# Kernel tuning notes

Measured on AMD Instinct MI355X. Metric: run time of the kernel, lower is better.

## Reference

```python
import jax, jax.numpy as jnp
import numpy as np

BS, L, D = 32, 512, 512
N_CHARS = 32
DICT = 97

def setup_inputs() -> dict:
    key = jax.random.key(0)
    ks = jax.random.split(key, 10)
    s = 1.0 / np.sqrt(D)
    return {
        "inp": jax.random.normal(ks[0], (BS, L, D), jnp.float32),
        "emb": jax.random.normal(ks[1], (N_CHARS, D), jnp.float32) * 0.02,  # embedding table; char_orders == arange
        "Wo_w": jax.random.normal(ks[2], (D, D), jnp.float32) * s,
        "Wo_b": jnp.zeros((D,), jnp.float32),
        "Wv_w": jax.random.normal(ks[3], (D, D), jnp.float32) * s,
        "Wv_b": jnp.zeros((D,), jnp.float32),
        "We_w": jax.random.normal(ks[4], (D, 1), jnp.float32) * s,
        "We_b": jnp.zeros((1,), jnp.float32),
        "Wc_w": jax.random.normal(ks[5], (D, DICT), jnp.float32) * s,
        "Wc_b": jnp.zeros((DICT,), jnp.float32),
    }

def reference(inp, emb, Wo_w, Wo_b, Wv_w, Wv_b, We_w, We_b, Wc_w, Wc_b):
    # O = embedding(arange(max_n_chars)) is just the full embedding table: (n, d)
    w_o = emb @ Wo_w + Wo_b                      # (n, d)
    w_v = inp @ Wv_w + Wv_b                      # (b, L, d)
    # broadcast add -> tanh -> score projection: (b, n, L, d) -> (b, n, L)
    h = jnp.tanh(w_o[None, :, None, :] + w_v[:, None, :, :])
    e = jnp.einsum('bnld,d->bnl', h, We_w[:, 0]) + We_b[0]
    alpha = jax.nn.softmax(e, axis=2)            # softmax over L (axis=2)
    visual_features = jnp.einsum('bnl,bld->bnd', alpha, inp)  # (b, n, d)
    logits = visual_features @ Wc_w + Wc_b       # (b, n, dict)
    return (visual_features, logits)
```

## Files before the change

### kernel.cpp

```cpp
#include <hip/hip_runtime.h>
#include <hip/hip_bf16.h>

#define BS    32
#define LSEQ  512
#define DIM   512
#define NCH   32
#define NDICT 97
#define CHB   16

#define TANH_SCALE 2.8853900817779268f

typedef __attribute__((ext_vector_type(8))) short bf16x8;
typedef __attribute__((ext_vector_type(4))) float f32x4;

#define GLDS16(gsrc, ldst) \
  __builtin_amdgcn_global_load_lds((const __attribute__((address_space(1))) void*)(gsrc), \
                                   (__attribute__((address_space(3))) void*)(ldst), 16, 0, 0)

__device__ __forceinline__ float sig_from_scaled(float xs) {
    float e2 = __builtin_amdgcn_exp2f(xs);
    return __builtin_amdgcn_rcpf(1.0f + e2);
}

__device__ __forceinline__ void split2u(float x0, float x1, unsigned& hp, unsigned& lp) {
    unsigned r0 = __float_as_uint(x0) + 0x8000u;
    unsigned r1 = __float_as_uint(x1) + 0x8000u;
    float f0 = __uint_as_float(r0 & 0xFFFF0000u);
    float f1 = __uint_as_float(r1 & 0xFFFF0000u);
    hp = (r0 >> 16) | (r1 & 0xFFFF0000u);
    unsigned s0 = __float_as_uint(x0 - f0);
    unsigned s1 = __float_as_uint(x1 - f1);
    lp = (s0 >> 16) | (s1 & 0xFFFF0000u);
}

__global__ __launch_bounds__(256) void k_misc(
    const float* __restrict__ Wv, ushort* __restrict__ BhiT, ushort* __restrict__ BloT,
    const float* __restrict__ Wo, ushort* __restrict__ WohiT, ushort* __restrict__ WoloT,
    const float* __restrict__ emb, ushort* __restrict__ embH, ushort* __restrict__ embL)
{
    __shared__ float tile[64][65];
    const int bid = blockIdx.x;
    const int t = threadIdx.x;
    if (bid < 128) {
        const bool isWv = bid < 64;
        const float* src = isWv ? Wv : Wo;
        ushort* dH = isWv ? BhiT : WohiT;
        ushort* dL = isWv ? BloT : WoloT;
        const int bb = bid & 63;
        const int k0 = (bb >> 3) * 64, n0 = (bb & 7) * 64;
        const int tr = t >> 4, tc = (t & 15) * 4;
        #pragma unroll
        for (int rr = 0; rr < 64; rr += 16) {
            float4 v = *(const float4*)&src[(size_t)(k0 + rr + tr) * DIM + n0 + tc];
            tile[rr + tr][tc + 0] = v.x; tile[rr + tr][tc + 1] = v.y;
            tile[rr + tr][tc + 2] = v.z; tile[rr + tr][tc + 3] = v.w;
        }
        __syncthreads();
        #pragma unroll
        for (int rr = 0; rr < 64; rr += 16) {
            const int n = rr + tr;
            unsigned h01, l01, h23, l23;
            split2u(tile[tc + 0][n] * TANH_SCALE, tile[tc + 1][n] * TANH_SCALE, h01, l01);
            split2u(tile[tc + 2][n] * TANH_SCALE, tile[tc + 3][n] * TANH_SCALE, h23, l23);
            *(uint2*)&dH[(size_t)(n0 + n) * DIM + k0 + tc] = make_uint2(h01, h23);
            *(uint2*)&dL[(size_t)(n0 + n) * DIM + k0 + tc] = make_uint2(l01, l23);
        }
    } else {
        for (int i = t; i < 4096; i += 256) {
            float4 v = ((const float4*)emb)[i];
            unsigned h01, l01, h23, l23;
            split2u(v.x, v.y, h01, l01);
            split2u(v.z, v.w, h23, l23);
            ((uint2*)embH)[i] = make_uint2(h01, h23);
            ((uint2*)embL)[i] = make_uint2(l01, l23);
        }
    }
}

__global__ __launch_bounds__(256) void k_gemm(
    const float* __restrict__ A,
    const ushort* __restrict__ Bhi, const ushort* __restrict__ Blo,
    const float* __restrict__ bias, float* __restrict__ C,
    const ushort* __restrict__ WohiT, const ushort* __restrict__ WoloT,
    const ushort* __restrict__ embH, const ushort* __restrict__ embL,
    const float* __restrict__ Wo_b, float* __restrict__ w_o)
{
    __shared__ ushort Bh[128 * 64], Bl[128 * 64];

    const int bid = blockIdx.x;
    const int t = threadIdx.x;
    const int wave = t >> 6, lane = t & 63;
    const int rl = lane >> 3;
    const int gsw = (lane & 7) ^ rl;

    if (bid < 512) {
        const int mb = (bid & 7) * 16 + (bid >> 5);
        const int nb = (bid >> 3) & 3;
        const int bm = mb * 128, bn = nb * 128;
        const int wm = wave >> 1, wn = wave & 1;
        const int am = bm + wm * 64 + (lane & 15);
        const int ak = (lane >> 4) * 8;

        f32x4 acc[4][4] = {};

        for (int k0 = 0; k0 < DIM; k0 += 64) {
            bf16x8 ah[4][2], al[4][2];
            #pragma unroll
            for (int i = 0; i < 4; ++i)
                #pragma unroll
                for (int kh = 0; kh < 2; ++kh) {
                    const float* ap = A + (size_t)(am + i * 16) * DIM + k0 + kh * 32 + ak;
                    float4 v0 = *(const float4*)ap;
                    float4 v1 = *(const float4*)(ap + 4);
                    union { unsigned u[4]; bf16x8 v; } H, L;
                    split2u(v0.x, v0.y, H.u[0], L.u[0]);
                    split2u(v0.z, v0.w, H.u[1], L.u[1]);
                    split2u(v1.x, v1.y, H.u[2], L.u[2]);
                    split2u(v1.z, v1.w, H.u[3], L.u[3]);
                    ah[i][kh] = H.v; al[i][kh] = L.v;
                }
            #pragma unroll
            for (int c4 = 0; c4 < 4; ++c4) {
                const int c = wave * 4 + c4;
                const size_t rb = (size_t)(bn + c * 8 + rl) * DIM + k0 + gsw * 8;
                GLDS16(Bhi + rb, &Bh[c * 512]);
                GLDS16(Blo + rb, &Bl[c * 512]);
            }
            __syncthreads();

            #pragma unroll
            for (int kh = 0; kh < 2; ++kh) {
                const int p = ((kh * 4 + (lane >> 4)) ^ (lane & 7)) * 8;
                bf16x8 bh[4], bl[4];
                #pragma unroll
                for (int j = 0; j < 4; ++j) {
                    const int rbr = (wn * 64 + j * 16 + (lane & 15)) * 64 + p;
                    bh[j] = *(const bf16x8*)&Bh[rbr];
                    bl[j] = *(const bf16x8*)&Bl[rbr];
                }
                #pragma unroll
                for (int i = 0; i < 4; ++i)
                    #pragma unroll
                    for (int j = 0; j < 4; ++j) {
                        acc[i][j] = __builtin_amdgcn_mfma_f32_16x16x32_bf16(ah[i][kh], bh[j], acc[i][j], 0, 0, 0);
                        acc[i][j] = __builtin_amdgcn_mfma_f32_16x16x32_bf16(ah[i][kh], bl[j], acc[i][j], 0, 0, 0);
                        acc[i][j] = __builtin_amdgcn_mfma_f32_16x16x32_bf16(al[i][kh], bh[j], acc[i][j], 0, 0, 0);
                    }
            }
            __syncthreads();
        }

        #pragma unroll
        for (int i = 0; i < 4; ++i) {
            const int m = bm + wm * 64 + i * 16 + (lane >> 4) * 4;
            #pragma unroll
            for (int j = 0; j < 4; ++j) {
                const int n = bn + wn * 64 + j * 16 + (lane & 15);
                const float bb = TANH_SCALE * bias[n];
                #pragma unroll
                for (int r = 0; r < 4; ++r)
                    C[(size_t)(m + r) * DIM + n] = acc[i][j][r] + bb;
            }
        }
    } else {
        const int nb0 = (bid - 512) * 128;
        f32x4 acc[2][2] = {};

        for (int k0 = 0; k0 < DIM; k0 += 64) {
            bf16x8 eh[2][2], el[2][2];
            #pragma unroll
            for (int m = 0; m < 2; ++m)
                #pragma unroll
                for (int kh = 0; kh < 2; ++kh) {
                    const size_t ra = (size_t)(m * 16 + (lane & 15)) * DIM + k0 + kh * 32 + (lane >> 4) * 8;
                    eh[m][kh] = *(const bf16x8*)&embH[ra];
                    el[m][kh] = *(const bf16x8*)&embL[ra];
                }
            #pragma unroll
            for (int c4 = 0; c4 < 4; ++c4) {
                const int c = wave * 4 + c4;
                const size_t rb = (size_t)(nb0 + c * 8 + rl) * DIM + k0 + gsw * 8;
                GLDS16(WohiT + rb, &Bh[c * 512]);
                GLDS16(WoloT + rb, &Bl[c * 512]);
            }
            __syncthreads();

            #pragma unroll
            for (int kh = 0; kh < 2; ++kh) {
                const int p = ((kh * 4 + (lane >> 4)) ^ (lane & 7)) * 8;
                bf16x8 bh[2], bl[2];
                #pragma unroll
                for (int j = 0; j < 2; ++j) {
                    const int rbr = (wave * 32 + j * 16 + (lane & 15)) * 64 + p;
                    bh[j] = *(const bf16x8*)&Bh[rbr];
                    bl[j] = *(const bf16x8*)&Bl[rbr];
                }
                #pragma unroll
                for (int m = 0; m < 2; ++m)
                    #pragma unroll
                    for (int j = 0; j < 2; ++j) {
                        acc[m][j] = __builtin_amdgcn_mfma_f32_16x16x32_bf16(eh[m][kh], bh[j], acc[m][j], 0, 0, 0);
                        acc[m][j] = __builtin_amdgcn_mfma_f32_16x16x32_bf16(eh[m][kh], bl[j], acc[m][j], 0, 0, 0);
                        acc[m][j] = __builtin_amdgcn_mfma_f32_16x16x32_bf16(el[m][kh], bh[j], acc[m][j], 0, 0, 0);
                    }
            }
            __syncthreads();
        }

        #pragma unroll
        for (int m = 0; m < 2; ++m) {
            const int row = m * 16 + (lane >> 4) * 4;
            #pragma unroll
            for (int j = 0; j < 2; ++j) {
                const int col = nb0 + wave * 32 + j * 16 + (lane & 15);
                const float bb = TANH_SCALE * Wo_b[col];
                #pragma unroll
                for (int r = 0; r < 4; ++r)
                    w_o[(size_t)(row + r) * DIM + col] = acc[m][j][r] + bb;
            }
        }
    }
}

__global__ __launch_bounds__(256, 4) void k_e(
    const float* __restrict__ w_v, const float* __restrict__ w_o,
    const float* __restrict__ We_w, float* __restrict__ e)
{
    __shared__ float4 woS[CHB * 128];
    const int lblk = blockIdx.x;
    const int b    = blockIdx.y;
    const int ch0  = blockIdx.z * CHB;
    const int t    = threadIdx.x;

    const float4* wog = ((const float4*)w_o) + ch0 * (DIM / 4);
    #pragma unroll
    for (int i = 0; i < CHB * 128 / 256; ++i)
        woS[t + 256 * i] = wog[t + 256 * i];

    const int wave = t >> 6, lane = t & 63;
    const int g = lane >> 4, j = lane & 15;
    const int l = lblk * 16 + wave * 4 + g;

    const float4* wvp = (const float4*)(w_v + (size_t)(b * LSEQ + l) * DIM);
    const float4* wep = (const float4*)We_w;
    float4 wv[8], we[8];
    #pragma unroll
    for (int k = 0; k < 8; ++k) {
        wv[k] = wvp[16 * k + j];
        we[k] = wep[16 * k + j];
    }
    float wsum = 0.0f;
    #pragma unroll
    for (int k = 0; k < 8; ++k)
        wsum += (we[k].x + we[k].y) + (we[k].z + we[k].w);
    #pragma unroll
    for (int off = 1; off < 16; off <<= 1) wsum += __shfl_xor(wsum, off, 64);

    __syncthreads();

    float sv[CHB];
    #pragma unroll 4
    for (int i = 0; i < CHB; ++i) {
        const float4* wrow = &woS[i * 128];
        float s0 = 0.f, s1 = 0.f, s2 = 0.f, s3 = 0.f;
        #pragma unroll
        for (int k = 0; k < 8; ++k) {
            float4 wo4 = wrow[16 * k + j];
            s0 = fmaf(we[k].x, sig_from_scaled(wo4.x + wv[k].x), s0);
            s1 = fmaf(we[k].y, sig_from_scaled(wo4.y + wv[k].y), s1);
            s2 = fmaf(we[k].z, sig_from_scaled(wo4.z + wv[k].z), s2);
            s3 = fmaf(we[k].w, sig_from_scaled(wo4.w + wv[k].w), s3);
        }
        sv[i] = (s0 + s1) + (s2 + s3);
    }

    float t2[8];
    #pragma unroll
    for (int i = 0; i < 8; ++i) {
        float a = sv[2 * i]     + __shfl_xor(sv[2 * i],     1, 64);
        float c = sv[2 * i + 1] + __shfl_xor(sv[2 * i + 1], 1, 64);
        t2[i] = (j & 1) ? c : a;
    }
    float t4[4];
    #pragma unroll
    for (int i = 0; i < 4; ++i) {
        float a = t2[2 * i]     + __shfl_xor(t2[2 * i],     2, 64);
        float c = t2[2 * i + 1] + __shfl_xor(t2[2 * i + 1], 2, 64);
        t4[i] = (j & 2) ? c : a;
    }
    float t8[2];
    #pragma unroll
    for (int i = 0; i < 2; ++i) {
        float a = t4[2 * i]     + __shfl_xor(t4[2 * i],     4, 64);
        float c = t4[2 * i + 1] + __shfl_xor(t4[2 * i + 1], 4, 64);
        t8[i] = (j & 4) ? c : a;
    }
    float a = t8[0] + __shfl_xor(t8[0], 8, 64);
    float c = t8[1] + __shfl_xor(t8[1], 8, 64);
    float res = (j & 8) ? c : a;

    e[(size_t)(b * NCH + ch0 + j) * LSEQ + l] = fmaf(-2.0f, res, wsum);
}

__global__ __launch_bounds__(256) void k_soft(
    const float* __restrict__ e, ushort* __restrict__ aH, ushort* __restrict__ aL)
{
    const int row = blockIdx.x * 4 + (threadIdx.x >> 6);
    const int lane = threadIdx.x & 63;
    const float4* erow = (const float4*)(e + (size_t)row * LSEQ);
    float4 v0 = erow[2 * lane], v1 = erow[2 * lane + 1];
    float m = fmaxf(fmaxf(fmaxf(v0.x, v0.y), fmaxf(v0.z, v0.w)),
                    fmaxf(fmaxf(v1.x, v1.y), fmaxf(v1.z, v1.w)));
    #pragma unroll
    for (int off = 32; off > 0; off >>= 1) m = fmaxf(m, __shfl_xor(m, off, 64));
    float p[8];
    p[0] = __expf(v0.x - m); p[1] = __expf(v0.y - m);
    p[2] = __expf(v0.z - m); p[3] = __expf(v0.w - m);
    p[4] = __expf(v1.x - m); p[5] = __expf(v1.y - m);
    p[6] = __expf(v1.z - m); p[7] = __expf(v1.w - m);
    float s = ((p[0] + p[1]) + (p[2] + p[3])) + ((p[4] + p[5]) + (p[6] + p[7]));
    #pragma unroll
    for (int off = 32; off > 0; off >>= 1) s += __shfl_xor(s, off, 64);
    const float inv = 1.0f / s;
    unsigned h01, l01, h23, l23, h45, l45, h67, l67;
    split2u(p[0] * inv, p[1] * inv, h01, l01);
    split2u(p[2] * inv, p[3] * inv, h23, l23);
    split2u(p[4] * inv, p[5] * inv, h45, l45);
    split2u(p[6] * inv, p[7] * inv, h67, l67);
    uint2* oh = (uint2*)(aH + (size_t)row * LSEQ);
    uint2* ol = (uint2*)(aL + (size_t)row * LSEQ);
    oh[2 * lane]     = make_uint2(h01, h23);
    oh[2 * lane + 1] = make_uint2(h45, h67);
    ol[2 * lane]     = make_uint2(l01, l23);
    ol[2 * lane + 1] = make_uint2(l45, l67);
}

__global__ __launch_bounds__(256) void k_vf(
    const float* __restrict__ inp,
    const ushort* __restrict__ aH, const ushort* __restrict__ aL,
    float* __restrict__ part)
{
    __shared__ unsigned T[4][16 * 68];
    const int dgrp = blockIdx.x >> 1, ls = blockIdx.x & 1;
    const int b = blockIdx.y;
    const int t = threadIdx.x, wave = t >> 6, lane = t & 63;
    const int d0 = (dgrp * 4 + wave) * 16;
    const int lbase = ls * 256;
    const int c = lane & 15, g = lane >> 4;

    unsigned* Tw = T[wave];
    const ushort* aHb = aH + (size_t)b * NCH * LSEQ;
    const ushort* aLb = aL + (size_t)b * NCH * LSEQ;

    f32x4 acc0 = {}, acc1 = {};

    for (int l0 = 0; l0 < 256; l0 += 64) {
        const float4* src = (const float4*)(inp + ((size_t)(b * LSEQ) + lbase + l0 + lane) * DIM + d0);
        float4 v0 = src[0], v1 = src[1], v2 = src[2], v3 = src[3];
        unsigned ev[16];
        {
            unsigned hp, lp;
            split2u(v0.x, v0.y, hp, lp); ev[0] = (lp << 16) | (hp & 0xFFFFu); ev[1] = (lp & 0xFFFF0000u) | (hp >> 16);
            split2u(v0.z, v0.w, hp, lp); ev[2] = (lp << 16) | (hp & 0xFFFFu); ev[3] = (lp & 0xFFFF0000u) | (hp >> 16);
            split2u(v1.x, v1.y, hp, lp); ev[4] = (lp << 16) | (hp & 0xFFFFu); ev[5] = (lp & 0xFFFF0000u) | (hp >> 16);
            split2u(v1.z, v1.w, hp, lp); ev[6] = (lp << 16) | (hp & 0xFFFFu); ev[7] = (lp & 0xFFFF0000u) | (hp >> 16);
            split2u(v2.x, v2.y, hp, lp); ev[8] = (lp << 16) | (hp & 0xFFFFu); ev[9] = (lp & 0xFFFF0000u) | (hp >> 16);
            split2u(v2.z, v2.w, hp, lp); ev[10] = (lp << 16) | (hp & 0xFFFFu); ev[11] = (lp & 0xFFFF0000u) | (hp >> 16);
            split2u(v3.x, v3.y, hp, lp); ev[12] = (lp << 16) | (hp & 0xFFFFu); ev[13] = (lp & 0xFFFF0000u) | (hp >> 16);
            split2u(v3.z, v3.w, hp, lp); ev[14] = (lp << 16) | (hp & 0xFFFFu); ev[15] = (lp & 0xFFFF0000u) | (hp >> 16);
        }
        #pragma unroll
        for (int i = 0; i < 16; ++i)
            Tw[i * 68 + lane] = ev[i];
        #pragma unroll
        for (int ks = 0; ks < 2; ++ks) {
            const unsigned* bp = &Tw[c * 68 + ks * 32 + g * 8];
            uint4 w0 = *(const uint4*)bp;
            uint4 w1 = *(const uint4*)(bp + 4);
            union { unsigned u[4]; bf16x8 v; } H, L;
            H.u[0] = (w0.x & 0xFFFFu) | (w0.y << 16);
            H.u[1] = (w0.z & 0xFFFFu) | (w0.w << 16);
            H.u[2] = (w1.x & 0xFFFFu) | (w1.y << 16);
            H.u[3] = (w1.z & 0xFFFFu) | (w1.w << 16);
            L.u[0] = (w0.x >> 16) | (w0.y & 0xFFFF0000u);
            L.u[1] = (w0.z >> 16) | (w0.w & 0xFFFF0000u);
            L.u[2] = (w1.x >> 16) | (w1.y & 0xFFFF0000u);
            L.u[3] = (w1.z >> 16) | (w1.w & 0xFFFF0000u);

            const int lfrag = lbase + l0 + ks * 32 + g * 8;
            bf16x8 a0h = *(const bf16x8*)&aHb[(size_t)c * LSEQ + lfrag];
            bf16x8 a0l = *(const bf16x8*)&aLb[(size_t)c * LSEQ + lfrag];
            bf16x8 a1h = *(const bf16x8*)&aHb[(size_t)(16 + c) * LSEQ + lfrag];
            bf16x8 a1l = *(const bf16x8*)&aLb[(size_t)(16 + c) * LSEQ + lfrag];

            acc0 = __builtin_amdgcn_mfma_f32_16x16x32_bf16(a0h, H.v, acc0, 0, 0, 0);
            acc0 = __builtin_amdgcn_mfma_f32_16x16x32_bf16(a0h, L.v, acc0, 0, 0, 0);
            acc0 = __builtin_amdgcn_mfma_f32_16x16x32_bf16(a0l, H.v, acc0, 0, 0, 0);
            acc1 = __builtin_amdgcn_mfma_f32_16x16x32_bf16(a1h, H.v, acc1, 0, 0, 0);
            acc1 = __builtin_amdgcn_mfma_f32_16x16x32_bf16(a1h, L.v, acc1, 0, 0, 0);
            acc1 = __builtin_amdgcn_mfma_f32_16x16x32_bf16(a1l, H.v, acc1, 0, 0, 0);
        }
    }

    const size_t base = (size_t)(ls * BS * NCH + b * NCH) * DIM + d0 + c;
    #pragma unroll
    for (int r = 0; r < 4; ++r) {
        part[base + (size_t)(g * 4 + r) * DIM]        = acc0[r];
        part[base + (size_t)(16 + g * 4 + r) * DIM]   = acc1[r];
    }
}

__global__ __launch_bounds__(256) void k_lg(
    const float* __restrict__ part, const float* __restrict__ Wc_w,
    const float* __restrict__ Wc_b, float* __restrict__ out_vf,
    float* __restrict__ out_logits)
{
    __shared__ float vfS[4][DIM];
    __shared__ float lgS[2][4][NDICT];
    const int r0 = blockIdx.x * 4;
    const int t = threadIdx.x;
    const int wave = t >> 6, lane = t & 63;

    const float2* p0 = (const float2*)(part + (size_t)(r0 + wave) * DIM);
    const float2* p1 = (const float2*)(part + (size_t)(BS * NCH + r0 + wave) * DIM);
    float2* vout = (float2*)(out_vf + (size_t)(r0 + wave) * DIM);
    #pragma unroll
    for (int q = 0; q < 4; ++q) {
        float2 x = p0[lane + 64 * q], y = p1[lane + 64 * q];
        float2 z; z.x = x.x + y.x; z.y = x.y + y.y;
        ((float2*)&vfS[wave][0])[lane + 64 * q] = z;
        vout[lane + 64 * q] = z;
    }
    __syncthreads();

    const int j = t & 127, half = t >> 7;
    if (j < NDICT) {
        const float* wc = Wc_w + (size_t)half * 256 * NDICT + j;
        const float* v0 = &vfS[0][half * 256];
        const float* v1 = &vfS[1][half * 256];
        const float* v2 = &vfS[2][half * 256];
        const float* v3 = &vfS[3][half * 256];
        float a0 = 0.f, a1 = 0.f, a2 = 0.f, a3 = 0.f;
        #pragma unroll 4
        for (int d = 0; d < 256; ++d) {
            float w = wc[(size_t)d * NDICT];
            a0 = fmaf(v0[d], w, a0); a1 = fmaf(v1[d], w, a1);
            a2 = fmaf(v2[d], w, a2); a3 = fmaf(v3[d], w, a3);
        }
        lgS[half][0][j] = a0; lgS[half][1][j] = a1;
        lgS[half][2][j] = a2; lgS[half][3][j] = a3;
    }
    __syncthreads();
    for (int idx = t; idx < 4 * NDICT; idx += 256) {
        const int r = idx / NDICT, jj = idx - r * NDICT;
        out_logits[(size_t)(r0 + r) * NDICT + jj] = Wc_b[jj] + lgS[0][r][jj] + lgS[1][r][jj];
    }
}

extern "C" void kernel_launch(void* const* d_in, const int* in_sizes, int n_in,
                              void* d_out, int out_size, void* d_ws, size_t ws_size,
                              hipStream_t stream)
{
    const float* inp  = (const float*)d_in[0];
    const float* emb  = (const float*)d_in[1];
    const float* Wo_w = (const float*)d_in[2];
    const float* Wo_b = (const float*)d_in[3];
    const float* Wv_w = (const float*)d_in[4];
    const float* Wv_b = (const float*)d_in[5];
    const float* We_w = (const float*)d_in[6];
    const float* Wc_w = (const float*)d_in[8];
    const float* Wc_b = (const float*)d_in[9];

    char* p = (char*)d_ws;
    float*  w_o   = (float*)p;  p += (64 << 10);
    float*  ev    = (float*)p;  p += (size_t)BS * NCH * LSEQ * 4;
    ushort* BhiT  = (ushort*)p; p += (size_t)DIM * DIM * 2;
    ushort* BloT  = (ushort*)p; p += (size_t)DIM * DIM * 2;
    ushort* WohiT = (ushort*)p; p += (size_t)DIM * DIM * 2;
    ushort* WoloT = (ushort*)p; p += (size_t)DIM * DIM * 2;
    ushort* embH  = (ushort*)p; p += (size_t)NCH * DIM * 2;
    ushort* embL  = (ushort*)p; p += (size_t)NCH * DIM * 2;
    ushort* aH    = (ushort*)p; p += (size_t)BS * NCH * LSEQ * 2;
    ushort* aL    = (ushort*)p; p += (size_t)BS * NCH * LSEQ * 2;
    float*  partV = (float*)p;  p += (size_t)2 * BS * NCH * DIM * 4;
    float*  w_v   = (float*)p;

    float* out_vf = (float*)d_out;
    float* out_lg = out_vf + BS * NCH * DIM;

    k_misc<<<dim3(129), dim3(256), 0, stream>>>(Wv_w, BhiT, BloT, Wo_w, WohiT, WoloT, emb, embH, embL);
    k_gemm<<<dim3(516), dim3(256), 0, stream>>>(inp, BhiT, BloT, Wv_b, w_v,
                                                WohiT, WoloT, embH, embL, Wo_b, w_o);
    k_e<<<dim3(LSEQ / 16, BS, NCH / CHB), dim3(256), 0, stream>>>(w_v, w_o, We_w, ev);
    k_soft<<<dim3(256), dim3(256), 0, stream>>>(ev, aH, aL);
    k_vf<<<dim3(16, BS), dim3(256), 0, stream>>>(inp, aH, aL, partV);
    k_lg<<<dim3(256), dim3(256), 0, stream>>>(partV, Wc_w, Wc_b, out_vf, out_lg);
}
```

Before: 175.1 us.

## Pre-split input into bf16 hi/lo planes and stage A tiles via LDS

Adds a separate kernel that splits the fp32 input into bf16 hi/lo arrays once. The GEMM then loads both A and B tiles into LDS with direct global-to-LDS loads and a new XOR swizzle, using a 32-wide K step instead of 64. This removes per-block fp32 loading and splitting of A, which was repeated across the four N-blocks, and moves A staging onto the async LDS path. In exchange it adds an extra pass that writes and re-reads about 32 MB of hi/lo data, and it halves the work done per barrier.

```diff
diff --git a/kernel.cpp b/kernel.cpp
--- a/kernel.cpp
+++ b/kernel.cpp
@@ -31,6 +31,22 @@
     unsigned s0 = __float_as_uint(x0 - f0);
     unsigned s1 = __float_as_uint(x1 - f1);
     lp = (s0 >> 16) | (s1 & 0xFFFF0000u);
+}
+
+__global__ __launch_bounds__(256) void k_prep_a(
+    const float* __restrict__ in, ushort* __restrict__ hi, ushort* __restrict__ lo)
+{
+    const int i0 = blockIdx.x * 1024 + threadIdx.x;
+    #pragma unroll
+    for (int rep = 0; rep < 4; ++rep) {
+        const int i = i0 + rep * 256;
+        float4 v = ((const float4*)in)[i];
+        unsigned h01, l01, h23, l23;
+        split2u(v.x, v.y, h01, l01);
+        split2u(v.z, v.w, h23, l23);
+        ((uint2*)hi)[i] = make_uint2(h01, h23);
+        ((uint2*)lo)[i] = make_uint2(l01, l23);
+    }
 }
 
 __global__ __launch_bounds__(256) void k_misc(
@@ -78,75 +94,64 @@
 }
 
 __global__ __launch_bounds__(256) void k_gemm(
-    const float* __restrict__ A,
+    const ushort* __restrict__ Ahi, const ushort* __restrict__ Alo,
     const ushort* __restrict__ Bhi, const ushort* __restrict__ Blo,
     const float* __restrict__ bias, float* __restrict__ C,
     const ushort* __restrict__ WohiT, const ushort* __restrict__ WoloT,
     const ushort* __restrict__ embH, const ushort* __restrict__ embL,
     const float* __restrict__ Wo_b, float* __restrict__ w_o)
 {
-    __shared__ ushort Bh[128 * 64], Bl[128 * 64];
+    __shared__ ushort AhS[4096], AlS[4096], BhS[4096], BlS[4096];
 
     const int bid = blockIdx.x;
     const int t = threadIdx.x;
     const int wave = t >> 6, lane = t & 63;
-    const int rl = lane >> 3;
-    const int gsw = (lane & 7) ^ rl;
+
+    const int srow = lane >> 2;
+    const int sg   = (lane & 3) ^ ((lane >> 3) & 3);
+
+    const int fr   = lane & 15;
+    const int fswz = ((lane >> 4) ^ ((fr >> 1) & 3)) * 8;
 
     if (bid < 512) {
         const int mb = (bid & 7) * 16 + (bid >> 5);
         const int nb = (bid >> 3) & 3;
         const int bm = mb * 128, bn = nb * 128;
         const int wm = wave >> 1, wn = wave & 1;
-        const int am = bm + wm * 64 + (lane & 15);
-        const int ak = (lane >> 4) * 8;
+        const int arow0 = (wm * 64 + fr) * 32;
+        const int brow0 = (wn * 64 + fr) * 32;
 
         f32x4 acc[4][4] = {};
 
-        for (int k0 = 0; k0 < DIM; k0 += 64) {
-            bf16x8 ah[4][2], al[4][2];
+        for (int k0 = 0; k0 < DIM; k0 += 32) {
+            #pragma unroll
+            for (int c2 = 0; c2 < 2; ++c2) {
+                const int c = wave * 2 + c2;
+                const size_t ga = (size_t)(bm + c * 16 + srow) * DIM + k0 + sg * 8;
+                const size_t gb = (size_t)(bn + c * 16 + srow) * DIM + k0 + sg * 8;
+                GLDS16(Ahi + ga, &AhS[c * 512]);
+                GLDS16(Alo + ga, &AlS[c * 512]);
+                GLDS16(Bhi + gb, &BhS[c * 512]);
+                GLDS16(Blo + gb, &BlS[c * 512]);
+            }
+            __syncthreads();
+
+            bf16x8 ah[4], al[4], bh[4], bl[4];
+            #pragma unroll
+            for (int i = 0; i < 4; ++i) {
+                ah[i] = *(const bf16x8*)&AhS[arow0 + i * 512 + fswz];
+                al[i] = *(const bf16x8*)&AlS[arow0 + i * 512 + fswz];
+                bh[i] = *(const bf16x8*)&BhS[brow0 + i * 512 + fswz];
+                bl[i] = *(const bf16x8*)&BlS[brow0 + i * 512 + fswz];
+            }
             #pragma unroll
             for (int i = 0; i < 4; ++i)
                 #pragma unroll
-                for (int kh = 0; kh < 2; ++kh) {
-                    const float* ap = A + (size_t)(am + i * 16) * DIM + k0 + kh * 32 + ak;
-                    float4 v0 = *(const float4*)ap;
-                    float4 v1 = *(const float4*)(ap + 4);
-                    union { unsigned u[4]; bf16x8 v; } H, L;
-                    split2u(v0.x, v0.y, H.u[0], L.u[0]);
-                    split2u(v0.z, v0.w, H.u[1], L.u[1]);
-                    split2u(v1.x, v1.y, H.u[2], L.u[2]);
-                    split2u(v1.z, v1.w, H.u[3], L.u[3]);
-                    ah[i][kh] = H.v; al[i][kh] = L.v;
+                for (int j = 0; j < 4; ++j) {
+                    acc[i][j] = __builtin_amdgcn_mfma_f32_16x16x32_bf16(ah[i], bh[j], acc[i][j], 0, 0, 0);
+                    acc[i][j] = __builtin_amdgcn_mfma_f32_16x16x32_bf16(ah[i], bl[j], acc[i][j], 0, 0, 0);
+                    acc[i][j] = __builtin_amdgcn_mfma_f32_16x16x32_bf16(al[i], bh[j], acc[i][j], 0, 0, 0);
                 }
-            #pragma unroll
-            for (int c4 = 0; c4 < 4; ++c4) {
-                const int c = wave * 4 + c4;
-                const size_t rb = (size_t)(bn + c * 8 + rl) * DIM + k0 + gsw * 8;
-                GLDS16(Bhi + rb, &Bh[c * 512]);
-                GLDS16(Blo + rb, &Bl[c * 512]);
-            }
-            __syncthreads();
-
-            #pragma unroll
-            for (int kh = 0; kh < 2; ++kh) {
-                const int p = ((kh * 4 + (lane >> 4)) ^ (lane & 7)) * 8;
-                bf16x8 bh[4], bl[4];
-                #pragma unroll
-                for (int j = 0; j < 4; ++j) {
-                    const int rbr = (wn * 64 + j * 16 + (lane & 15)) * 64 + p;
-                    bh[j] = *(const bf16x8*)&Bh[rbr];
-                    bl[j] = *(const bf16x8*)&Bl[rbr];
-                }
-                #pragma unroll
-                for (int i = 0; i < 4; ++i)
-                    #pragma unroll
-                    for (int j = 0; j < 4; ++j) {
-                        acc[i][j] = __builtin_amdgcn_mfma_f32_16x16x32_bf16(ah[i][kh], bh[j], acc[i][j], 0, 0, 0);
-                        acc[i][j] = __builtin_amdgcn_mfma_f32_16x16x32_bf16(ah[i][kh], bl[j], acc[i][j], 0, 0, 0);
-                        acc[i][j] = __builtin_amdgcn_mfma_f32_16x16x32_bf16(al[i][kh], bh[j], acc[i][j], 0, 0, 0);
-                    }
-            }
             __syncthreads();
         }
 
@@ -155,7 +160,7 @@
             const int m = bm + wm * 64 + i * 16 + (lane >> 4) * 4;
             #pragma unroll
             for (int j = 0; j < 4; ++j) {
-                const int n = bn + wn * 64 + j * 16 + (lane & 15);
+                const int n = bn + wn * 64 + j * 16 + fr;
                 const float bb = TANH_SCALE * bias[n];
                 #pragma unroll
                 for (int r = 0; r < 4; ++r)
@@ -164,46 +169,41 @@
         }
     } else {
         const int nb0 = (bid - 512) * 128;
+        const int crow0 = (wave * 32 + fr) * 32;
         f32x4 acc[2][2] = {};
 
-        for (int k0 = 0; k0 < DIM; k0 += 64) {
-            bf16x8 eh[2][2], el[2][2];
+        for (int k0 = 0; k0 < DIM; k0 += 32) {
+            #pragma unroll
+            for (int c4 = 0; c4 < 4; ++c4) {
+                const int idx = wave * 4 + c4;
+                const int pl = idx & 1, c = idx >> 1;
+                const size_t gb = (size_t)(nb0 + c * 16 + srow) * DIM + k0 + sg * 8;
+                if (pl) { GLDS16(WoloT + gb, &BlS[c * 512]); }
+                else    { GLDS16(WohiT + gb, &BhS[c * 512]); }
+            }
+            bf16x8 eh[2], el[2];
+            #pragma unroll
+            for (int m = 0; m < 2; ++m) {
+                const size_t ra = (size_t)(m * 16 + fr) * DIM + k0 + (lane >> 4) * 8;
+                eh[m] = *(const bf16x8*)&embH[ra];
+                el[m] = *(const bf16x8*)&embL[ra];
+            }
+            __syncthreads();
+
+            bf16x8 bh[2], bl[2];
+            #pragma unroll
+            for (int j = 0; j < 2; ++j) {
+                bh[j] = *(const bf16x8*)&BhS[crow0 + j * 512 + fswz];
+                bl[j] = *(const bf16x8*)&BlS[crow0 + j * 512 + fswz];
+            }
             #pragma unroll
             for (int m = 0; m < 2; ++m)
                 #pragma unroll
-                for (int kh = 0; kh < 2; ++kh) {
-                    const size_t ra = (size_t)(m * 16 + (lane & 15)) * DIM + k0 + kh * 32 + (lane >> 4) * 8;
-                    eh[m][kh] = *(const bf16x8*)&embH[ra];
-                    el[m][kh] = *(const bf16x8*)&embL[ra];
+                for (int j = 0; j < 2; ++j) {
+                    acc[m][j] = __builtin_amdgcn_mfma_f32_16x16x32_bf16(eh[m], bh[j], acc[m][j], 0, 0, 0);
+                    acc[m][j] = __builtin_amdgcn_mfma_f32_16x16x32_bf16(eh[m], bl[j], acc[m][j], 0, 0, 0);
+                    acc[m][j] = __builtin_amdgcn_mfma_f32_16x16x32_bf16(el[m], bh[j], acc[m][j], 0, 0, 0);
                 }
-            #pragma unroll
-            for (int c4 = 0; c4 < 4; ++c4) {
-                const int c = wave * 4 + c4;
-                const size_t rb = (size_t)(nb0 + c * 8 + rl) * DIM + k0 + gsw * 8;
-                GLDS16(WohiT + rb, &Bh[c * 512]);
-                GLDS16(WoloT + rb, &Bl[c * 512]);
-            }
-            __syncthreads();
-
-            #pragma unroll
-            for (int kh = 0; kh < 2; ++kh) {
-                const int p = ((kh * 4 + (lane >> 4)) ^ (lane & 7)) * 8;
-                bf16x8 bh[2], bl[2];
-                #pragma unroll
-                for (int j = 0; j < 2; ++j) {
-                    const int rbr = (wave * 32 + j * 16 + (lane & 15)) * 64 + p;
-                    bh[j] = *(const bf16x8*)&Bh[rbr];
-                    bl[j] = *(const bf16x8*)&Bl[rbr];
-                }
-                #pragma unroll
-                for (int m = 0; m < 2; ++m)
-                    #pragma unroll
-                    for (int j = 0; j < 2; ++j) {
-                        acc[m][j] = __builtin_amdgcn_mfma_f32_16x16x32_bf16(eh[m][kh], bh[j], acc[m][j], 0, 0, 0);
-                        acc[m][j] = __builtin_amdgcn_mfma_f32_16x16x32_bf16(eh[m][kh], bl[j], acc[m][j], 0, 0, 0);
-                        acc[m][j] = __builtin_amdgcn_mfma_f32_16x16x32_bf16(el[m][kh], bh[j], acc[m][j], 0, 0, 0);
-                    }
-            }
             __syncthreads();
         }
 
@@ -212,7 +212,7 @@
             const int row = m * 16 + (lane >> 4) * 4;
             #pragma unroll
             for (int j = 0; j < 2; ++j) {
-                const int col = nb0 + wave * 32 + j * 16 + (lane & 15);
+                const int col = nb0 + wave * 32 + j * 16 + fr;
                 const float bb = TANH_SCALE * Wo_b[col];
                 #pragma unroll
                 for (int r = 0; r < 4; ++r)
@@ -483,13 +483,16 @@
     ushort* aH    = (ushort*)p; p += (size_t)BS * NCH * LSEQ * 2;
     ushort* aL    = (ushort*)p; p += (size_t)BS * NCH * LSEQ * 2;
     float*  partV = (float*)p;  p += (size_t)2 * BS * NCH * DIM * 4;
+    ushort* Ahi   = (ushort*)p; p += (size_t)BS * LSEQ * DIM * 2;
+    ushort* Alo   = (ushort*)p; p += (size_t)BS * LSEQ * DIM * 2;
     float*  w_v   = (float*)p;
 
     float* out_vf = (float*)d_out;
     float* out_lg = out_vf + BS * NCH * DIM;
 
+    k_prep_a<<<dim3(2048), dim3(256), 0, stream>>>(inp, Ahi, Alo);
     k_misc<<<dim3(129), dim3(256), 0, stream>>>(Wv_w, BhiT, BloT, Wo_w, WohiT, WoloT, emb, embH, embL);
-    k_gemm<<<dim3(516), dim3(256), 0, stream>>>(inp, BhiT, BloT, Wv_b, w_v,
+    k_gemm<<<dim3(516), dim3(256), 0, stream>>>(Ahi, Alo, BhiT, BloT, Wv_b, w_v,
                                                 WohiT, WoloT, embH, embL, Wo_b, w_o);
     k_e<<<dim3(LSEQ / 16, BS, NCH / CHB), dim3(256), 0, stream>>>(w_v, w_o, We_w, ev);
     k_soft<<<dim3(256), dim3(256), 0, stream>>>(ev, aH, aL);
```

Result: faster. 152.9 us (-12.7%).
